# Kernel tuning notes

Measured on AMD Instinct MI355X. Metric: run time of the kernel, lower is better.

The kernel has to match this reference:

```python
import jax, jax.numpy as jnp
import numpy as np

N_NODES = 50000


def _cluster_gcn_conv(x, row, col, W_out, b_out, W_root, num_nodes):
    # PyG ClusterGCNConv with diag_lambda=0.0 and self-loops already added.
    deg = jax.ops.segment_sum(jnp.ones_like(col, dtype=x.dtype), col,
                              num_segments=num_nodes)
    deg_inv = 1.0 / jnp.clip(deg, 1.0)
    w = deg_inv[col]                       # [E_total]
    msg = x[row] * w[:, None]              # [E_total, d] gather + scale
    agg = jax.ops.segment_sum(msg, col, num_segments=num_nodes)  # scatter-add
    return agg @ W_out + b_out + x @ W_root


def setup_inputs() -> dict:
    key = jax.random.key(0)
    ks = jax.random.split(key, 12)
    N, E, d_in, d_h, d_out = N_NODES, 800000, 128, 128, 64
    x = jax.random.normal(ks[0], (N, d_in), dtype=jnp.float32)
    edge_index = jax.random.randint(ks[1], (2, E), 0, N, dtype=jnp.int64)
    s = lambda fan_in: 1.0 / np.sqrt(fan_in)
    return {
        "x": x,
        "edge_index": edge_index,
        "W1_out": jax.random.normal(ks[2], (d_in, d_h), jnp.float32) * s(d_in),
        "b1": jnp.zeros((d_h,), jnp.float32),
        "W1_root": jax.random.normal(ks[3], (d_in, d_h), jnp.float32) * s(d_in),
        "W2_out": jax.random.normal(ks[4], (d_h, d_h), jnp.float32) * s(d_h),
        "b2": jnp.zeros((d_h,), jnp.float32),
        "W2_root": jax.random.normal(ks[5], (d_h, d_h), jnp.float32) * s(d_h),
        "W3_out": jax.random.normal(ks[6], (d_h, d_out), jnp.float32) * s(d_h),
        "b3": jnp.zeros((d_out,), jnp.float32),
        "W3_root": jax.random.normal(ks[7], (d_h, d_out), jnp.float32) * s(d_h),
    }


def reference(x, edge_index, W1_out, b1, W1_root, W2_out, b2, W2_root,
              W3_out, b3, W3_root):
    N = x.shape[0]
    loops = jnp.arange(N, dtype=edge_index.dtype)
    row = jnp.concatenate([edge_index[0], loops])  # add self loops
    col = jnp.concatenate([edge_index[1], loops])
    # layer 1 + relu (dropout is identity at inference)
    x = jax.nn.relu(_cluster_gcn_conv(x, row, col, W1_out, b1, W1_root, N))
    # layer 2 + relu
    x = jax.nn.relu(_cluster_gcn_conv(x, row, col, W2_out, b2, W2_root, N))
    # layer 3 + relu, then log_softmax (no pooling: node classification)
    x = jax.nn.relu(_cluster_gcn_conv(x, row, col, W3_out, b3, W3_root, N))
    return jax.nn.log_softmax(x, axis=-1)
```

## Files before the change

kernel.cpp:

```cpp
#include <hip/hip_runtime.h>
#include <math.h>


constexpr int DK = 128;
constexpr int NBUCK = 256;

typedef __attribute__((ext_vector_type(8))) short bf16x8;
typedef __attribute__((ext_vector_type(4))) float f32x4;

__device__ inline unsigned short f2bf(float f) {
    unsigned int u; __builtin_memcpy(&u, &f, 4);
    unsigned int r = (u + 0x7FFFu + ((u >> 16) & 1u)) >> 16;
    return (unsigned short)r;
}
__device__ inline float blo(unsigned int u) {
    unsigned int t = u << 16; float f; __builtin_memcpy(&f, &t, 4); return f;
}
__device__ inline float bhi(unsigned int u) {
    unsigned int t = u & 0xffff0000u; float f; __builtin_memcpy(&f, &t, 4); return f;
}

__device__ void wprep_body(const float* __restrict__ Wout, const float* __restrict__ Wroot,
                           uint4* __restrict__ frag, int dout, int tid) {
    int total = 8 * (dout >> 4) * 64;
    if (tid >= total) return;
    int L = tid & 63;
    int fu = (tid >> 6) % (dout >> 4);
    int t = (tid >> 6) / (dout >> 4);
    int quad = L >> 4, l15 = L & 15;
    int n = fu * 16 + l15;
    unsigned int p[4];
#pragma unroll
    for (int jj = 0; jj < 4; ++jj) {
        int k0 = t * 32 + quad * 8 + jj * 2;
        float v0 = (k0 < 128) ? Wout[k0 * dout + n] : Wroot[(k0 - 128) * dout + n];
        int k1 = k0 + 1;
        float v1 = (k1 < 128) ? Wout[k1 * dout + n] : Wroot[(k1 - 128) * dout + n];
        p[jj] = (unsigned)f2bf(v0) | ((unsigned)f2bf(v1) << 16);
    }
    frag[tid] = make_uint4(p[0], p[1], p[2], p[3]);
}

__global__ void k_prep(const float4* __restrict__ x, uint2* __restrict__ xb,
                       int* __restrict__ bhist, const int* __restrict__ col,
                       int n4, int E, int bspan,
                       const float* __restrict__ W1o, const float* __restrict__ W1r, uint4* wf1,
                       const float* __restrict__ W2o, const float* __restrict__ W2r, uint4* wf2,
                       const float* __restrict__ W3o, const float* __restrict__ W3r, uint4* wf3) {
    const int nxblk = (n4 + 255) / 256;
    const int b = blockIdx.x;
    const int tid = threadIdx.x;
    if (b < nxblk) {
        int i = b * 256 + tid;
        if (i >= n4) return;
        float4 v = x[i];
        uint2 o;
        o.x = (unsigned)f2bf(v.x) | ((unsigned)f2bf(v.y) << 16);
        o.y = (unsigned)f2bf(v.z) | ((unsigned)f2bf(v.w) << 16);
        xb[i] = o;
    } else if (b < nxblk + 16) {
        wprep_body(W1o, W1r, wf1, 128, (b - nxblk) * 256 + tid);
    } else if (b < nxblk + 32) {
        wprep_body(W2o, W2r, wf2, 128, (b - nxblk - 16) * 256 + tid);
    } else if (b < nxblk + 40) {
        wprep_body(W3o, W3r, wf3, 64, (b - nxblk - 32) * 256 + tid);
    } else {
        __shared__ int h[NBUCK];
        h[tid] = 0;
        __syncthreads();
        for (int i = (b - nxblk - 40) * 256 + tid; i < E; i += 400 * 256)
            atomicAdd(&h[col[i] / bspan], 1);
        __syncthreads();
        int v = h[tid];
        if (v) atomicAdd(&bhist[tid], v);
    }
}

__global__ void k_part(const int* __restrict__ row, const int* __restrict__ col,
                       const int* __restrict__ bhist, int* __restrict__ bcur0,
                       unsigned int* __restrict__ ebuf, int e, int bspan) {
    __shared__ int cnt[NBUCK];
    __shared__ int base[NBUCK];
    __shared__ int wsum[4];
    const int tid = threadIdx.x, lane = tid & 63, wid = tid >> 6;
    int v = bhist[tid];
    int ps = v;
#pragma unroll
    for (int off = 1; off < 64; off <<= 1) {
        int t = __shfl_up(ps, off);
        if (lane >= off) ps += t;
    }
    if (lane == 63) wsum[wid] = ps;
    __syncthreads();
    int wb = 0;
    for (int w = 0; w < wid; ++w) wb += wsum[w];
    const int excl = wb + ps - v;

    const int t0 = blockIdx.x * 4096;
    cnt[tid] = 0;
    __syncthreads();
    int bk[16];
#pragma unroll
    for (int k = 0; k < 16; ++k) {
        int i = t0 + k * 256 + tid;
        int b = -1;
        if (i < e) { b = col[i] / bspan; atomicAdd(&cnt[b], 1); }
        bk[k] = b;
    }
    __syncthreads();
    base[tid] = excl + (cnt[tid] ? atomicAdd(&bcur0[tid], cnt[tid]) : 0);
    cnt[tid] = 0;
    __syncthreads();
#pragma unroll
    for (int k = 0; k < 16; ++k) {
        int i = t0 + k * 256 + tid;
        if (i < e) {
            int b = bk[k];
            int slot = base[b] + atomicAdd(&cnt[b], 1);
            unsigned int colofs = (unsigned)(col[i] - b * bspan);
            ebuf[slot] = ((unsigned)row[i] & 0xFFFFu) | (colofs << 16);
        }
    }
}

__global__ void k_fillb(const unsigned int* __restrict__ ebuf,
                        const int* __restrict__ bhist, int* __restrict__ offs,
                        float* __restrict__ deginv, unsigned short* __restrict__ srow,
                        int n, int e, int bspan) {
    __shared__ int cnt[4096];
    __shared__ int scan_s[NBUCK + 1];
    __shared__ int wsum[4];
    const int b = blockIdx.x, tid = threadIdx.x;
    const int lane = tid & 63, wid = tid >> 6;
    {
        int v = bhist[tid];
        int ps = v;
#pragma unroll
        for (int off = 1; off < 64; off <<= 1) {
            int t = __shfl_up(ps, off);
            if (lane >= off) ps += t;
        }
        if (lane == 63) wsum[wid] = ps;
        __syncthreads();
        int wb = 0;
        for (int w = 0; w < wid; ++w) wb += wsum[w];
        int excl = wb + ps - v;
        scan_s[tid] = excl;
        if (tid == 255) scan_s[256] = excl + v;
    }
    for (int i = tid; i < 4096; i += 256) cnt[i] = 0;
    __syncthreads();
    const int start = scan_s[b], end = scan_s[b + 1];
    if (b == NBUCK - 1 && tid == 0) offs[n] = e;
    for (int i = start + tid; i < end; i += 256) {
        const unsigned u = ebuf[i];
        atomicAdd(&cnt[(int)(u >> 16) * 16 + (int)((u & 0xFFFFu) >> 12)], 1);
    }
    __syncthreads();
    int v[16], s = 0;
#pragma unroll
    for (int r = 0; r < 16; ++r) { v[r] = cnt[tid * 16 + r]; s += v[r]; }
    int ps = s;
#pragma unroll
    for (int off = 1; off < 64; off <<= 1) {
        int t = __shfl_up(ps, off);
        if (lane >= off) ps += t;
    }
    if (lane == 63) wsum[wid] = ps;
    __syncthreads();
    int wb = 0;
    for (int w = 0; w < wid; ++w) wb += wsum[w];
    int excl = start + wb + ps - s;
    const int node = b * bspan + tid;
    if (tid < bspan && node < n) {
        offs[node] = excl;
        deginv[node] = 1.0f / (float)(s + 1);
    }
#pragma unroll
    for (int r = 0; r < 16; ++r) { int t = v[r]; cnt[tid * 16 + r] = excl; excl += t; }
    __syncthreads();
    for (int i = start + tid; i < end; i += 256) {
        const unsigned u = ebuf[i];
        const int pos = atomicAdd(&cnt[(int)(u >> 16) * 16 + (int)((u & 0xFFFFu) >> 12)], 1);
        srow[pos] = (unsigned short)(u & 0xFFFFu);
    }
}

template <bool HR>
__global__ __launch_bounds__(256, 5)
void k_fused(const unsigned short* __restrict__ xb,
             const int* __restrict__ offs, const unsigned short* __restrict__ srow,
             const float* __restrict__ deginv,
             const uint4* __restrict__ wfrag, const float* __restrict__ bvec,
             unsigned short* __restrict__ y,
             const uint4* __restrict__ wfrag3, const float* __restrict__ b3,
             unsigned short* __restrict__ H, float* __restrict__ R, int n) {
    __shared__ unsigned short At[32][136];
    const int tid = threadIdx.x;
    const int m0 = blockIdx.x * 32;
    const uint4* __restrict__ xb4 = (const uint4*)xb;

#pragma unroll
    for (int rnd = 0; rnd < 2; ++rnd) {
        const int nl = rnd * 16 + (tid >> 4);
        const int lane = tid & 15;
        const int node = m0 + nl;
        if (node < n) {
            const size_t rb = (size_t)node * 16 + lane;
            uint4 sv = xb4[rb];
            float a0 = blo(sv.x), a1 = bhi(sv.x), a2 = blo(sv.y), a3 = bhi(sv.y);
            float a4 = blo(sv.z), a5 = bhi(sv.z), a6 = blo(sv.w), a7 = bhi(sv.w);
            const int s = offs[node], e = offs[node + 1];
            int p = s;
            for (; p + 4 <= e; p += 4) {
                const int r0 = srow[p], r1 = srow[p + 1];
                const int r2 = srow[p + 2], r3 = srow[p + 3];
                const uint4 v0 = xb4[(size_t)r0 * 16 + lane];
                const uint4 v1 = xb4[(size_t)r1 * 16 + lane];
                const uint4 v2 = xb4[(size_t)r2 * 16 + lane];
                const uint4 v3 = xb4[(size_t)r3 * 16 + lane];
                a0 += (blo(v0.x) + blo(v1.x)) + (blo(v2.x) + blo(v3.x));
                a1 += (bhi(v0.x) + bhi(v1.x)) + (bhi(v2.x) + bhi(v3.x));
                a2 += (blo(v0.y) + blo(v1.y)) + (blo(v2.y) + blo(v3.y));
                a3 += (bhi(v0.y) + bhi(v1.y)) + (bhi(v2.y) + bhi(v3.y));
                a4 += (blo(v0.z) + blo(v1.z)) + (blo(v2.z) + blo(v3.z));
                a5 += (bhi(v0.z) + bhi(v1.z)) + (bhi(v2.z) + bhi(v3.z));
                a6 += (blo(v0.w) + blo(v1.w)) + (blo(v2.w) + blo(v3.w));
                a7 += (bhi(v0.w) + bhi(v1.w)) + (bhi(v2.w) + bhi(v3.w));
            }
            for (; p < e; ++p) {
                const uint4 v = xb4[(size_t)srow[p] * 16 + lane];
                a0 += blo(v.x); a1 += bhi(v.x); a2 += blo(v.y); a3 += bhi(v.y);
                a4 += blo(v.z); a5 += bhi(v.z); a6 += blo(v.w); a7 += bhi(v.w);
            }
            const float w = deginv[node];
            uint4 o;
            o.x = (unsigned)f2bf(a0 * w) | ((unsigned)f2bf(a1 * w) << 16);
            o.y = (unsigned)f2bf(a2 * w) | ((unsigned)f2bf(a3 * w) << 16);
            o.z = (unsigned)f2bf(a4 * w) | ((unsigned)f2bf(a5 * w) << 16);
            o.w = (unsigned)f2bf(a6 * w) | ((unsigned)f2bf(a7 * w) << 16);
            *(uint4*)&At[nl][lane * 8] = o;
        }
    }
    __syncthreads();

    const int w = tid >> 6, L = tid & 63;
    const int quad = L >> 4, l15 = L & 15;

    f32x4 acc[2][2];
#pragma unroll
    for (int mt = 0; mt < 2; ++mt)
#pragma unroll
        for (int u = 0; u < 2; ++u)
            acc[mt][u] = (f32x4){0.f, 0.f, 0.f, 0.f};

    const bf16x8 zf = {0, 0, 0, 0, 0, 0, 0, 0};
#pragma unroll
    for (int t = 0; t < 8; ++t) {
        bf16x8 bfr[2];
#pragma unroll
        for (int u = 0; u < 2; ++u)
            bfr[u] = *(const bf16x8*)&wfrag[(size_t)((t * 8 + (w * 2 + u)) * 64 + L)];
        const int koff = (t & 3) * 32 + quad * 8;
        bf16x8 af[2];
#pragma unroll
        for (int mt = 0; mt < 2; ++mt) {
            const int rl = mt * 16 + l15;
            if (t < 4) {
                af[mt] = *(const bf16x8*)&At[rl][koff];
            } else {
                const int r = m0 + rl;
                af[mt] = (r < n) ? *(const bf16x8*)(xb + (size_t)r * 128 + koff) : zf;
            }
        }
#pragma unroll
        for (int mt = 0; mt < 2; ++mt)
#pragma unroll
            for (int u = 0; u < 2; ++u)
                acc[mt][u] = __builtin_amdgcn_mfma_f32_16x16x32_bf16(
                    af[mt], bfr[u], acc[mt][u], 0, 0, 0);
    }

    float bb[2];
    bb[0] = bvec[w * 32 + l15];
    bb[1] = bvec[w * 32 + 16 + l15];

    if (!HR) {
#pragma unroll
        for (int mt = 0; mt < 2; ++mt)
#pragma unroll
            for (int u = 0; u < 2; ++u)
#pragma unroll
                for (int r4 = 0; r4 < 4; ++r4) {
                    const int r = m0 + mt * 16 + quad * 4 + r4;
                    if (r < n) {
                        float v = fmaxf(acc[mt][u][r4] + bb[u], 0.f);
                        y[(size_t)r * 128 + w * 32 + u * 16 + l15] = f2bf(v);
                    }
                }
        return;
    }

    __syncthreads();
#pragma unroll
    for (int mt = 0; mt < 2; ++mt)
#pragma unroll
        for (int u = 0; u < 2; ++u)
#pragma unroll
            for (int r4 = 0; r4 < 4; ++r4) {
                const int rl = mt * 16 + quad * 4 + r4;
                float v = fmaxf(acc[mt][u][r4] + bb[u], 0.f);
                At[rl][w * 32 + u * 16 + l15] = f2bf(v);
            }
    __syncthreads();

    f32x4 accH[2], accR[2];
#pragma unroll
    for (int mt = 0; mt < 2; ++mt) {
        accH[mt] = (f32x4){0.f, 0.f, 0.f, 0.f};
        accR[mt] = (f32x4){0.f, 0.f, 0.f, 0.f};
    }
#pragma unroll
    for (int t = 0; t < 4; ++t) {
        const bf16x8 bo = *(const bf16x8*)&wfrag3[(size_t)((t * 4 + w) * 64 + L)];
        const bf16x8 br = *(const bf16x8*)&wfrag3[(size_t)(((t + 4) * 4 + w) * 64 + L)];
        const int koff = t * 32 + quad * 8;
        bf16x8 af[2];
#pragma unroll
        for (int mt = 0; mt < 2; ++mt)
            af[mt] = *(const bf16x8*)&At[mt * 16 + l15][koff];
#pragma unroll
        for (int mt = 0; mt < 2; ++mt) {
            accH[mt] = __builtin_amdgcn_mfma_f32_16x16x32_bf16(af[mt], bo, accH[mt], 0, 0, 0);
            accR[mt] = __builtin_amdgcn_mfma_f32_16x16x32_bf16(af[mt], br, accR[mt], 0, 0, 0);
        }
    }
    const float bb3 = b3[w * 16 + l15];
#pragma unroll
    for (int mt = 0; mt < 2; ++mt)
#pragma unroll
        for (int r4 = 0; r4 < 4; ++r4) {
            const int r = m0 + mt * 16 + quad * 4 + r4;
            if (r < n) {
                H[(size_t)r * 64 + w * 16 + l15] = f2bf(accH[mt][r4]);
                R[(size_t)r * 64 + w * 16 + l15] = accR[mt][r4] + bb3;
            }
        }
}

__global__ __launch_bounds__(256, 8)
void k_gather3(const uint2* __restrict__ Hb, const float4* __restrict__ R4,
               const int* __restrict__ offs, const unsigned short* __restrict__ srow,
               const float* __restrict__ deginv, float4* __restrict__ out, int n) {
    const int node = blockIdx.x * 16 + (threadIdx.x >> 4);
    const int lane = threadIdx.x & 15;
    if (node >= n) return;
    const size_t rb = (size_t)node * 16 + lane;
    uint2 sv = Hb[rb];
    float a0 = blo(sv.x), a1 = bhi(sv.x), a2 = blo(sv.y), a3 = bhi(sv.y);
    const int s = offs[node], e = offs[node + 1];
    int p = s;
    for (; p + 4 <= e; p += 4) {
        const int r0 = srow[p], r1 = srow[p + 1], r2 = srow[p + 2], r3 = srow[p + 3];
        const uint2 v0 = Hb[(size_t)r0 * 16 + lane];
        const uint2 v1 = Hb[(size_t)r1 * 16 + lane];
        const uint2 v2 = Hb[(size_t)r2 * 16 + lane];
        const uint2 v3 = Hb[(size_t)r3 * 16 + lane];
        a0 += (blo(v0.x) + blo(v1.x)) + (blo(v2.x) + blo(v3.x));
        a1 += (bhi(v0.x) + bhi(v1.x)) + (bhi(v2.x) + bhi(v3.x));
        a2 += (blo(v0.y) + blo(v1.y)) + (blo(v2.y) + blo(v3.y));
        a3 += (bhi(v0.y) + bhi(v1.y)) + (bhi(v2.y) + bhi(v3.y));
    }
    for (; p < e; ++p) {
        const uint2 v = Hb[(size_t)srow[p] * 16 + lane];
        a0 += blo(v.x); a1 += bhi(v.x); a2 += blo(v.y); a3 += bhi(v.y);
    }
    const float w = deginv[node];
    const float4 r = R4[rb];
    float v0 = fmaxf(a0 * w + r.x, 0.f);
    float v1 = fmaxf(a1 * w + r.y, 0.f);
    float v2 = fmaxf(a2 * w + r.z, 0.f);
    float v3 = fmaxf(a3 * w + r.w, 0.f);
    float m = fmaxf(fmaxf(v0, v1), fmaxf(v2, v3));
    m = fmaxf(m, __shfl_xor(m, 1));
    m = fmaxf(m, __shfl_xor(m, 2));
    m = fmaxf(m, __shfl_xor(m, 4));
    m = fmaxf(m, __shfl_xor(m, 8));
    float s2 = __expf(v0 - m) + __expf(v1 - m) + __expf(v2 - m) + __expf(v3 - m);
    s2 += __shfl_xor(s2, 1);
    s2 += __shfl_xor(s2, 2);
    s2 += __shfl_xor(s2, 4);
    s2 += __shfl_xor(s2, 8);
    const float lse = m + __logf(s2);
    out[rb] = make_float4(v0 - lse, v1 - lse, v2 - lse, v3 - lse);
}

extern "C" void kernel_launch(void* const* d_in, const int* in_sizes, int n_in,
                              void* d_out, int out_size, void* d_ws, size_t ws_size,
                              hipStream_t stream) {
    const float* x   = (const float*)d_in[0];
    const int*   ei  = (const int*)d_in[1];
    const float* W1o = (const float*)d_in[2];
    const float* b1  = (const float*)d_in[3];
    const float* W1r = (const float*)d_in[4];
    const float* W2o = (const float*)d_in[5];
    const float* b2  = (const float*)d_in[6];
    const float* W2r = (const float*)d_in[7];
    const float* W3o = (const float*)d_in[8];
    const float* b3  = (const float*)d_in[9];
    const float* W3r = (const float*)d_in[10];

    const int N = in_sizes[0] / DK;
    const int E = in_sizes[1] / 2;
    const int* row = ei;
    const int* col = ei + E;
    const int bspan = (N + NBUCK - 1) / NBUCK;

    int*   bhist  = (int*)d_ws;
    int*   bcur0  = bhist + 256;
    int*   offs   = bcur0 + 256;
    float* deginv = (float*)(offs + ((N + 64) & ~63));
    unsigned short* srow = (unsigned short*)(deginv + ((N + 63) & ~63));
    unsigned int* ebuf = (unsigned int*)(srow + ((E + 63) & ~63));
    uint4* wf1    = (uint4*)(ebuf + ((E + 63) & ~63));
    uint4* wf2    = wf1 + 4096;
    uint4* wf3    = wf2 + 4096;
    unsigned short* xbuf = (unsigned short*)(wf3 + 2048);
    unsigned short* Ya   = xbuf + (size_t)N * 128;
    unsigned short* Hb   = Ya + (size_t)N * 128;
    float* Rb = (float*)(Hb + (size_t)N * 64);
    float* out = (float*)d_out;

    const int n4 = N * 32;
    const int nxblk = (n4 + 255) / 256;

    hipMemsetAsync(bhist, 0, 512 * sizeof(int), stream);
    k_prep<<<nxblk + 440, 256, 0, stream>>>((const float4*)x, (uint2*)xbuf, bhist, col,
                                            n4, E, bspan,
                                            W1o, W1r, wf1, W2o, W2r, wf2, W3o, W3r, wf3);

    k_part<<<(E + 4095) / 4096, 256, 0, stream>>>(row, col, bhist, bcur0, ebuf, E, bspan);
    k_fillb<<<NBUCK, 256, 0, stream>>>(ebuf, bhist, offs, deginv, srow, N, E, bspan);

    const int Gf = (N + 31) / 32;
    const int Gg3 = (N + 15) / 16;

    k_fused<false><<<Gf, 256, 0, stream>>>(xbuf, offs, srow, deginv, wf1, b1, Ya,
                                           nullptr, nullptr, nullptr, nullptr, N);
    k_fused<true><<<Gf, 256, 0, stream>>>(Ya, offs, srow, deginv, wf2, b2, nullptr,
                                          wf3, b3, Hb, Rb, N);
    k_gather3<<<Gg3, 256, 0, stream>>>((const uint2*)Hb, (const float4*)Rb,
                                       offs, srow, deginv, (float4*)out, N);
}
```

Before: 229.3 us.

## Store node features in column-sliced layout to shrink gather working set

```diff
diff --git a/kernel.cpp b/kernel.cpp
--- a/kernel.cpp
+++ b/kernel.cpp
@@ -43,7 +43,7 @@
 
 __global__ void k_prep(const float4* __restrict__ x, uint2* __restrict__ xb,
                        int* __restrict__ bhist, const int* __restrict__ col,
-                       int n4, int E, int bspan,
+                       int n4, int N, int E, int bspan,
                        const float* __restrict__ W1o, const float* __restrict__ W1r, uint4* wf1,
                        const float* __restrict__ W2o, const float* __restrict__ W2r, uint4* wf2,
                        const float* __restrict__ W3o, const float* __restrict__ W3r, uint4* wf3) {
@@ -51,13 +51,14 @@
     const int b = blockIdx.x;
     const int tid = threadIdx.x;
     if (b < nxblk) {
-        int i = b * 256 + tid;
-        if (i >= n4) return;
-        float4 v = x[i];
+        int j = b * 256 + tid;
+        if (j >= n4) return;
+        float4 v = x[j];
+        int node = j >> 5, c = j & 31;
         uint2 o;
         o.x = (unsigned)f2bf(v.x) | ((unsigned)f2bf(v.y) << 16);
         o.y = (unsigned)f2bf(v.z) | ((unsigned)f2bf(v.w) << 16);
-        xb[i] = o;
+        xb[((size_t)(c >> 3) * N + node) * 8 + (c & 7)] = o;
     } else if (b < nxblk + 16) {
         wprep_body(W1o, W1r, wf1, 128, (b - nxblk) * 256 + tid);
     } else if (b < nxblk + 32) {
@@ -198,48 +199,43 @@
     __shared__ unsigned short At[32][136];
     const int tid = threadIdx.x;
     const int m0 = blockIdx.x * 32;
-    const uint4* __restrict__ xb4 = (const uint4*)xb;
-
-#pragma unroll
-    for (int rnd = 0; rnd < 2; ++rnd) {
-        const int nl = rnd * 16 + (tid >> 4);
-        const int lane = tid & 15;
+    const uint2* __restrict__ xb2 = (const uint2*)xb;
+
+    {
+        const int nl = tid >> 3;
+        const int lane = tid & 7;
         const int node = m0 + nl;
-        if (node < n) {
-            const size_t rb = (size_t)node * 16 + lane;
-            uint4 sv = xb4[rb];
-            float a0 = blo(sv.x), a1 = bhi(sv.x), a2 = blo(sv.y), a3 = bhi(sv.y);
-            float a4 = blo(sv.z), a5 = bhi(sv.z), a6 = blo(sv.w), a7 = bhi(sv.w);
-            const int s = offs[node], e = offs[node + 1];
-            int p = s;
-            for (; p + 4 <= e; p += 4) {
-                const int r0 = srow[p], r1 = srow[p + 1];
-                const int r2 = srow[p + 2], r3 = srow[p + 3];
-                const uint4 v0 = xb4[(size_t)r0 * 16 + lane];
-                const uint4 v1 = xb4[(size_t)r1 * 16 + lane];
-                const uint4 v2 = xb4[(size_t)r2 * 16 + lane];
-                const uint4 v3 = xb4[(size_t)r3 * 16 + lane];
-                a0 += (blo(v0.x) + blo(v1.x)) + (blo(v2.x) + blo(v3.x));
-                a1 += (bhi(v0.x) + bhi(v1.x)) + (bhi(v2.x) + bhi(v3.x));
-                a2 += (blo(v0.y) + blo(v1.y)) + (blo(v2.y) + blo(v3.y));
-                a3 += (bhi(v0.y) + bhi(v1.y)) + (bhi(v2.y) + bhi(v3.y));
-                a4 += (blo(v0.z) + blo(v1.z)) + (blo(v2.z) + blo(v3.z));
-                a5 += (bhi(v0.z) + bhi(v1.z)) + (bhi(v2.z) + bhi(v3.z));
-                a6 += (blo(v0.w) + blo(v1.w)) + (blo(v2.w) + blo(v3.w));
-                a7 += (bhi(v0.w) + bhi(v1.w)) + (bhi(v2.w) + bhi(v3.w));
+        int se = 0, ee = 0;
+        float wdeg = 0.f;
+        if (node < n) { se = offs[node]; ee = offs[node + 1]; wdeg = deginv[node]; }
+#pragma unroll 1
+        for (int sl = 0; sl < 4; ++sl) {
+            if (node < n) {
+                const uint2* __restrict__ xsl = xb2 + (size_t)sl * n * 8;
+                uint2 sv = xsl[(size_t)node * 8 + lane];
+                float a0 = blo(sv.x), a1 = bhi(sv.x), a2 = blo(sv.y), a3 = bhi(sv.y);
+                int p = se;
+                for (; p + 4 <= ee; p += 4) {
+                    const int r0 = srow[p], r1 = srow[p + 1];
+                    const int r2 = srow[p + 2], r3 = srow[p + 3];
+                    const uint2 v0 = xsl[(size_t)r0 * 8 + lane];
+                    const uint2 v1 = xsl[(size_t)r1 * 8 + lane];
+                    const uint2 v2 = xsl[(size_t)r2 * 8 + lane];
+                    const uint2 v3 = xsl[(size_t)r3 * 8 + lane];
+                    a0 += (blo(v0.x) + blo(v1.x)) + (blo(v2.x) + blo(v3.x));
+                    a1 += (bhi(v0.x) + bhi(v1.x)) + (bhi(v2.x) + bhi(v3.x));
+                    a2 += (blo(v0.y) + blo(v1.y)) + (blo(v2.y) + blo(v3.y));
+                    a3 += (bhi(v0.y) + bhi(v1.y)) + (bhi(v2.y) + bhi(v3.y));
+                }
+                for (; p < ee; ++p) {
+                    const uint2 v = xsl[(size_t)srow[p] * 8 + lane];
+                    a0 += blo(v.x); a1 += bhi(v.x); a2 += blo(v.y); a3 += bhi(v.y);
+                }
+                uint2 o;
+                o.x = (unsigned)f2bf(a0 * wdeg) | ((unsigned)f2bf(a1 * wdeg) << 16);
+                o.y = (unsigned)f2bf(a2 * wdeg) | ((unsigned)f2bf(a3 * wdeg) << 16);
+                *(uint2*)&At[nl][sl * 32 + lane * 4] = o;
             }
-            for (; p < e; ++p) {
-                const uint4 v = xb4[(size_t)srow[p] * 16 + lane];
-                a0 += blo(v.x); a1 += bhi(v.x); a2 += blo(v.y); a3 += bhi(v.y);
-                a4 += blo(v.z); a5 += bhi(v.z); a6 += blo(v.w); a7 += bhi(v.w);
-            }
-            const float w = deginv[node];
-            uint4 o;
-            o.x = (unsigned)f2bf(a0 * w) | ((unsigned)f2bf(a1 * w) << 16);
-            o.y = (unsigned)f2bf(a2 * w) | ((unsigned)f2bf(a3 * w) << 16);
-            o.z = (unsigned)f2bf(a4 * w) | ((unsigned)f2bf(a5 * w) << 16);
-            o.w = (unsigned)f2bf(a6 * w) | ((unsigned)f2bf(a7 * w) << 16);
-            *(uint4*)&At[nl][lane * 8] = o;
         }
     }
     __syncthreads();
@@ -261,16 +257,17 @@
 #pragma unroll
         for (int u = 0; u < 2; ++u)
             bfr[u] = *(const bf16x8*)&wfrag[(size_t)((t * 8 + (w * 2 + u)) * 64 + L)];
-        const int koff = (t & 3) * 32 + quad * 8;
+        const int sl = t & 3;
         bf16x8 af[2];
 #pragma unroll
         for (int mt = 0; mt < 2; ++mt) {
             const int rl = mt * 16 + l15;
             if (t < 4) {
-                af[mt] = *(const bf16x8*)&At[rl][koff];
+                af[mt] = *(const bf16x8*)&At[rl][sl * 32 + quad * 8];
             } else {
                 const int r = m0 + rl;
-                af[mt] = (r < n) ? *(const bf16x8*)(xb + (size_t)r * 128 + koff) : zf;
+                af[mt] = (r < n) ? *(const bf16x8*)(xb + ((size_t)sl * n + r) * 32 + quad * 8)
+                                 : zf;
             }
         }
 #pragma unroll
@@ -295,7 +292,7 @@
                     const int r = m0 + mt * 16 + quad * 4 + r4;
                     if (r < n) {
                         float v = fmaxf(acc[mt][u][r4] + bb[u], 0.f);
-                        y[(size_t)r * 128 + w * 32 + u * 16 + l15] = f2bf(v);
+                        y[((size_t)w * n + r) * 32 + u * 16 + l15] = f2bf(v);
                     }
                 }
         return;
@@ -342,7 +339,7 @@
         for (int r4 = 0; r4 < 4; ++r4) {
             const int r = m0 + mt * 16 + quad * 4 + r4;
             if (r < n) {
-                H[(size_t)r * 64 + w * 16 + l15] = f2bf(accH[mt][r4]);
+                H[((size_t)(w >> 1) * n + r) * 32 + (w & 1) * 16 + l15] = f2bf(accH[mt][r4]);
                 R[(size_t)r * 64 + w * 16 + l15] = accR[mt][r4] + bb3;
             }
         }
@@ -352,47 +349,80 @@
 void k_gather3(const uint2* __restrict__ Hb, const float4* __restrict__ R4,
                const int* __restrict__ offs, const unsigned short* __restrict__ srow,
                const float* __restrict__ deginv, float4* __restrict__ out, int n) {
-    const int node = blockIdx.x * 16 + (threadIdx.x >> 4);
-    const int lane = threadIdx.x & 15;
+    const int node = blockIdx.x * 32 + (threadIdx.x >> 3);
+    const int lane = threadIdx.x & 7;
     if (node >= n) return;
-    const size_t rb = (size_t)node * 16 + lane;
-    uint2 sv = Hb[rb];
-    float a0 = blo(sv.x), a1 = bhi(sv.x), a2 = blo(sv.y), a3 = bhi(sv.y);
     const int s = offs[node], e = offs[node + 1];
-    int p = s;
-    for (; p + 4 <= e; p += 4) {
-        const int r0 = srow[p], r1 = srow[p + 1], r2 = srow[p + 2], r3 = srow[p + 3];
-        const uint2 v0 = Hb[(size_t)r0 * 16 + lane];
-        const uint2 v1 = Hb[(size_t)r1 * 16 + lane];
-        const uint2 v2 = Hb[(size_t)r2 * 16 + lane];
-        const uint2 v3 = Hb[(size_t)r3 * 16 + lane];
-        a0 += (blo(v0.x) + blo(v1.x)) + (blo(v2.x) + blo(v3.x));
-        a1 += (bhi(v0.x) + bhi(v1.x)) + (bhi(v2.x) + bhi(v3.x));
-        a2 += (blo(v0.y) + blo(v1.y)) + (blo(v2.y) + blo(v3.y));
-        a3 += (bhi(v0.y) + bhi(v1.y)) + (bhi(v2.y) + bhi(v3.y));
-    }
-    for (; p < e; ++p) {
-        const uint2 v = Hb[(size_t)srow[p] * 16 + lane];
-        a0 += blo(v.x); a1 += bhi(v.x); a2 += blo(v.y); a3 += bhi(v.y);
-    }
     const float w = deginv[node];
-    const float4 r = R4[rb];
-    float v0 = fmaxf(a0 * w + r.x, 0.f);
-    float v1 = fmaxf(a1 * w + r.y, 0.f);
-    float v2 = fmaxf(a2 * w + r.z, 0.f);
-    float v3 = fmaxf(a3 * w + r.w, 0.f);
-    float m = fmaxf(fmaxf(v0, v1), fmaxf(v2, v3));
+
+    float a0, a1, a2, a3;
+    {
+        const uint2* __restrict__ Hs = Hb;
+        uint2 sv = Hs[(size_t)node * 8 + lane];
+        a0 = blo(sv.x); a1 = bhi(sv.x); a2 = blo(sv.y); a3 = bhi(sv.y);
+        int p = s;
+        for (; p + 4 <= e; p += 4) {
+            const int r0 = srow[p], r1 = srow[p + 1], r2 = srow[p + 2], r3 = srow[p + 3];
+            const uint2 v0 = Hs[(size_t)r0 * 8 + lane];
+            const uint2 v1 = Hs[(size_t)r1 * 8 + lane];
+            const uint2 v2 = Hs[(size_t)r2 * 8 + lane];
+            const uint2 v3 = Hs[(size_t)r3 * 8 + lane];
+            a0 += (blo(v0.x) + blo(v1.x)) + (blo(v2.x) + blo(v3.x));
+            a1 += (bhi(v0.x) + bhi(v1.x)) + (bhi(v2.x) + bhi(v3.x));
+            a2 += (blo(v0.y) + blo(v1.y)) + (blo(v2.y) + blo(v3.y));
+            a3 += (bhi(v0.y) + bhi(v1.y)) + (bhi(v2.y) + bhi(v3.y));
+        }
+        for (; p < e; ++p) {
+            const uint2 v = Hs[(size_t)srow[p] * 8 + lane];
+            a0 += blo(v.x); a1 += bhi(v.x); a2 += blo(v.y); a3 += bhi(v.y);
+        }
+    }
+    float b0, b1, b2, b3;
+    {
+        const uint2* __restrict__ Hs = Hb + (size_t)n * 8;
+        uint2 sv = Hs[(size_t)node * 8 + lane];
+        b0 = blo(sv.x); b1 = bhi(sv.x); b2 = blo(sv.y); b3 = bhi(sv.y);
+        int p = s;
+        for (; p + 4 <= e; p += 4) {
+            const int r0 = srow[p], r1 = srow[p + 1], r2 = srow[p + 2], r3 = srow[p + 3];
+            const uint2 v0 = Hs[(size_t)r0 * 8 + lane];
+            const uint2 v1 = Hs[(size_t)r1 * 8 + lane];
+            const uint2 v2 = Hs[(size_t)r2 * 8 + lane];
+            const uint2 v3 = Hs[(size_t)r3 * 8 + lane];
+            b0 += (blo(v0.x) + blo(v1.x)) + (blo(v2.x) + blo(v3.x));
+            b1 += (bhi(v0.x) + bhi(v1.x)) + (bhi(v2.x) + bhi(v3.x));
+            b2 += (blo(v0.y) + blo(v1.y)) + (blo(v2.y) + blo(v3.y));
+            b3 += (bhi(v0.y) + bhi(v1.y)) + (bhi(v2.y) + bhi(v3.y));
+        }
+        for (; p < e; ++p) {
+            const uint2 v = Hs[(size_t)srow[p] * 8 + lane];
+            b0 += blo(v.x); b1 += bhi(v.x); b2 += blo(v.y); b3 += bhi(v.y);
+        }
+    }
+
+    const float4 r0 = R4[(size_t)node * 16 + lane];
+    const float4 r1 = R4[(size_t)node * 16 + 8 + lane];
+    float v0 = fmaxf(a0 * w + r0.x, 0.f);
+    float v1 = fmaxf(a1 * w + r0.y, 0.f);
+    float v2 = fmaxf(a2 * w + r0.z, 0.f);
+    float v3 = fmaxf(a3 * w + r0.w, 0.f);
+    float v4 = fmaxf(b0 * w + r1.x, 0.f);
+    float v5 = fmaxf(b1 * w + r1.y, 0.f);
+    float v6 = fmaxf(b2 * w + r1.z, 0.f);
+    float v7 = fmaxf(b3 * w + r1.w, 0.f);
+    float m = fmaxf(fmaxf(fmaxf(v0, v1), fmaxf(v2, v3)),
+                    fmaxf(fmaxf(v4, v5), fmaxf(v6, v7)));
     m = fmaxf(m, __shfl_xor(m, 1));
     m = fmaxf(m, __shfl_xor(m, 2));
     m = fmaxf(m, __shfl_xor(m, 4));
-    m = fmaxf(m, __shfl_xor(m, 8));
-    float s2 = __expf(v0 - m) + __expf(v1 - m) + __expf(v2 - m) + __expf(v3 - m);
+    float s2 = (__expf(v0 - m) + __expf(v1 - m)) + (__expf(v2 - m) + __expf(v3 - m)) +
+               (__expf(v4 - m) + __expf(v5 - m)) + (__expf(v6 - m) + __expf(v7 - m));
     s2 += __shfl_xor(s2, 1);
     s2 += __shfl_xor(s2, 2);
     s2 += __shfl_xor(s2, 4);
-    s2 += __shfl_xor(s2, 8);
     const float lse = m + __logf(s2);
-    out[rb] = make_float4(v0 - lse, v1 - lse, v2 - lse, v3 - lse);
+    out[(size_t)node * 16 + lane]     = make_float4(v0 - lse, v1 - lse, v2 - lse, v3 - lse);
+    out[(size_t)node * 16 + 8 + lane] = make_float4(v4 - lse, v5 - lse, v6 - lse, v7 - lse);
 }
 
 extern "C" void kernel_launch(void* const* d_in, const int* in_sizes, int n_in,
@@ -436,14 +466,14 @@
 
     hipMemsetAsync(bhist, 0, 512 * sizeof(int), stream);
     k_prep<<<nxblk + 440, 256, 0, stream>>>((const float4*)x, (uint2*)xbuf, bhist, col,
-                                            n4, E, bspan,
+                                            n4, N, E, bspan,
                                             W1o, W1r, wf1, W2o, W2r, wf2, W3o, W3r, wf3);
 
     k_part<<<(E + 4095) / 4096, 256, 0, stream>>>(row, col, bhist, bcur0, ebuf, E, bspan);
     k_fillb<<<NBUCK, 256, 0, stream>>>(ebuf, bhist, offs, deginv, srow, N, E, bspan);
 
     const int Gf = (N + 31) / 32;
-    const int Gg3 = (N + 15) / 16;
+    const int Gg3 = (N + 31) / 32;
 
     k_fused<false><<<Gf, 256, 0, stream>>>(xbuf, offs, srow, deginv, wf1, b1, Ya,
                                            nullptr, nullptr, nullptr, nullptr, N);
```

After: 241.5 us. +5.3%, slower.

## Double k_fused block to 512 threads, one node per thread group

Applied to the files above, without the earlier changes.

```diff
diff --git a/kernel.cpp b/kernel.cpp
--- a/kernel.cpp
+++ b/kernel.cpp
@@ -187,7 +187,7 @@
 }
 
 template <bool HR>
-__global__ __launch_bounds__(256, 5)
+__global__ __launch_bounds__(512, 8)
 void k_fused(const unsigned short* __restrict__ xb,
              const int* __restrict__ offs, const unsigned short* __restrict__ srow,
              const float* __restrict__ deginv,
@@ -200,9 +200,8 @@
     const int m0 = blockIdx.x * 32;
     const uint4* __restrict__ xb4 = (const uint4*)xb;
 
-#pragma unroll
-    for (int rnd = 0; rnd < 2; ++rnd) {
-        const int nl = rnd * 16 + (tid >> 4);
+    {
+        const int nl = tid >> 4;
         const int lane = tid & 15;
         const int node = m0 + nl;
         if (node < n) {
@@ -247,20 +246,14 @@
     const int w = tid >> 6, L = tid & 63;
     const int quad = L >> 4, l15 = L & 15;
 
-    f32x4 acc[2][2];
-#pragma unroll
-    for (int mt = 0; mt < 2; ++mt)
-#pragma unroll
-        for (int u = 0; u < 2; ++u)
-            acc[mt][u] = (f32x4){0.f, 0.f, 0.f, 0.f};
+    f32x4 acc[2];
+    acc[0] = (f32x4){0.f, 0.f, 0.f, 0.f};
+    acc[1] = (f32x4){0.f, 0.f, 0.f, 0.f};
 
     const bf16x8 zf = {0, 0, 0, 0, 0, 0, 0, 0};
 #pragma unroll
     for (int t = 0; t < 8; ++t) {
-        bf16x8 bfr[2];
-#pragma unroll
-        for (int u = 0; u < 2; ++u)
-            bfr[u] = *(const bf16x8*)&wfrag[(size_t)((t * 8 + (w * 2 + u)) * 64 + L)];
+        const bf16x8 bfr = *(const bf16x8*)&wfrag[(size_t)((t * 8 + w) * 64 + L)];
         const int koff = (t & 3) * 32 + quad * 8;
         bf16x8 af[2];
 #pragma unroll
@@ -275,29 +268,22 @@
         }
 #pragma unroll
         for (int mt = 0; mt < 2; ++mt)
-#pragma unroll
-            for (int u = 0; u < 2; ++u)
-                acc[mt][u] = __builtin_amdgcn_mfma_f32_16x16x32_bf16(
-                    af[mt], bfr[u], acc[mt][u], 0, 0, 0);
-    }
-
-    float bb[2];
-    bb[0] = bvec[w * 32 + l15];
-    bb[1] = bvec[w * 32 + 16 + l15];
+            acc[mt] = __builtin_amdgcn_mfma_f32_16x16x32_bf16(af[mt], bfr, acc[mt], 0, 0, 0);
+    }
+
+    const float bb = bvec[w * 16 + l15];
 
     if (!HR) {
 #pragma unroll
         for (int mt = 0; mt < 2; ++mt)
 #pragma unroll
-            for (int u = 0; u < 2; ++u)
-#pragma unroll
-                for (int r4 = 0; r4 < 4; ++r4) {
-                    const int r = m0 + mt * 16 + quad * 4 + r4;
-                    if (r < n) {
-                        float v = fmaxf(acc[mt][u][r4] + bb[u], 0.f);
-                        y[(size_t)r * 128 + w * 32 + u * 16 + l15] = f2bf(v);
-                    }
+            for (int r4 = 0; r4 < 4; ++r4) {
+                const int r = m0 + mt * 16 + quad * 4 + r4;
+                if (r < n) {
+                    float v = fmaxf(acc[mt][r4] + bb, 0.f);
+                    y[(size_t)r * 128 + w * 16 + l15] = f2bf(v);
                 }
+            }
         return;
     }
 
@@ -305,47 +291,46 @@
 #pragma unroll
     for (int mt = 0; mt < 2; ++mt)
 #pragma unroll
-        for (int u = 0; u < 2; ++u)
+        for (int r4 = 0; r4 < 4; ++r4) {
+            const int rl = mt * 16 + quad * 4 + r4;
+            float v = fmaxf(acc[mt][r4] + bb, 0.f);
+            At[rl][w * 16 + l15] = f2bf(v);
+        }
+    __syncthreads();
+
+    const int isR = (w >> 2) & 1;
+    const int fu = w & 3;
+    f32x4 accO[2];
+    accO[0] = (f32x4){0.f, 0.f, 0.f, 0.f};
+    accO[1] = (f32x4){0.f, 0.f, 0.f, 0.f};
+#pragma unroll
+    for (int t = 0; t < 4; ++t) {
+        const bf16x8 bf = *(const bf16x8*)&wfrag3[(size_t)(((t + isR * 4) * 4 + fu) * 64 + L)];
+        const int koff = t * 32 + quad * 8;
+#pragma unroll
+        for (int mt = 0; mt < 2; ++mt) {
+            const bf16x8 af = *(const bf16x8*)&At[mt * 16 + l15][koff];
+            accO[mt] = __builtin_amdgcn_mfma_f32_16x16x32_bf16(af, bf, accO[mt], 0, 0, 0);
+        }
+    }
+    if (!isR) {
+#pragma unroll
+        for (int mt = 0; mt < 2; ++mt)
 #pragma unroll
             for (int r4 = 0; r4 < 4; ++r4) {
-                const int rl = mt * 16 + quad * 4 + r4;
-                float v = fmaxf(acc[mt][u][r4] + bb[u], 0.f);
-                At[rl][w * 32 + u * 16 + l15] = f2bf(v);
-            }
-    __syncthreads();
-
-    f32x4 accH[2], accR[2];
-#pragma unroll
-    for (int mt = 0; mt < 2; ++mt) {
-        accH[mt] = (f32x4){0.f, 0.f, 0.f, 0.f};
-        accR[mt] = (f32x4){0.f, 0.f, 0.f, 0.f};
-    }
-#pragma unroll
-    for (int t = 0; t < 4; ++t) {
-        const bf16x8 bo = *(const bf16x8*)&wfrag3[(size_t)((t * 4 + w) * 64 + L)];
-        const bf16x8 br = *(const bf16x8*)&wfrag3[(size_t)(((t + 4) * 4 + w) * 64 + L)];
-        const int koff = t * 32 + quad * 8;
-        bf16x8 af[2];
+                const int r = m0 + mt * 16 + quad * 4 + r4;
+                if (r < n) H[(size_t)r * 64 + fu * 16 + l15] = f2bf(accO[mt][r4]);
+            }
+    } else {
+        const float bb3 = b3[fu * 16 + l15];
 #pragma unroll
         for (int mt = 0; mt < 2; ++mt)
-            af[mt] = *(const bf16x8*)&At[mt * 16 + l15][koff];
-#pragma unroll
-        for (int mt = 0; mt < 2; ++mt) {
-            accH[mt] = __builtin_amdgcn_mfma_f32_16x16x32_bf16(af[mt], bo, accH[mt], 0, 0, 0);
-            accR[mt] = __builtin_amdgcn_mfma_f32_16x16x32_bf16(af[mt], br, accR[mt], 0, 0, 0);
-        }
-    }
-    const float bb3 = b3[w * 16 + l15];
-#pragma unroll
-    for (int mt = 0; mt < 2; ++mt)
-#pragma unroll
-        for (int r4 = 0; r4 < 4; ++r4) {
-            const int r = m0 + mt * 16 + quad * 4 + r4;
-            if (r < n) {
-                H[(size_t)r * 64 + w * 16 + l15] = f2bf(accH[mt][r4]);
-                R[(size_t)r * 64 + w * 16 + l15] = accR[mt][r4] + bb3;
-            }
-        }
+#pragma unroll
+            for (int r4 = 0; r4 < 4; ++r4) {
+                const int r = m0 + mt * 16 + quad * 4 + r4;
+                if (r < n) R[(size_t)r * 64 + fu * 16 + l15] = accO[mt][r4] + bb3;
+            }
+    }
 }
 
 __global__ __launch_bounds__(256, 8)
@@ -445,9 +430,9 @@
     const int Gf = (N + 31) / 32;
     const int Gg3 = (N + 15) / 16;
 
-    k_fused<false><<<Gf, 256, 0, stream>>>(xbuf, offs, srow, deginv, wf1, b1, Ya,
+    k_fused<false><<<Gf, 512, 0, stream>>>(xbuf, offs, srow, deginv, wf1, b1, Ya,
                                            nullptr, nullptr, nullptr, nullptr, N);
-    k_fused<true><<<Gf, 256, 0, stream>>>(Ya, offs, srow, deginv, wf2, b2, nullptr,
+    k_fused<true><<<Gf, 512, 0, stream>>>(Ya, offs, srow, deginv, wf2, b2, nullptr,
                                           wf3, b3, Hb, Rb, N);
     k_gather3<<<Gg3, 256, 0, stream>>>((const uint2*)Hb, (const float4*)Rb,
                                        offs, srow, deginv, (float4*)out, N);
```

Result: slower. 240.1 us (+4.7%).
